# Kernel optimization log

Measured on AMD Instinct MI355X. Metric: run time of the kernel, lower is better.

## Reference

```python
import jax, jax.numpy as jnp
import numpy as np

N = 50000; FIN = 64; H = 128; E = 800000; T = 8
P = 250000; D = 500000; G = 20000; V = 2000; O = 2


def _mp(h, Ws, Wn, b, edge_src, edge_dst, n):
    # mean-aggregation message passing: relu(h Ws + mean_neigh(h) Wn + b)
    deg = jax.ops.segment_sum(jnp.ones(edge_dst.shape[0], h.dtype), edge_dst, n)
    agg = jax.ops.segment_sum(h[edge_src], edge_dst, n) / jnp.maximum(deg, 1.0)[:, None]
    return jax.nn.relu(h @ Ws + agg @ Wn + b)


def _forward(x, W_enc_self, W_enc_nei, b_enc, W2_self, W2_nei, b2, Wd1, bd1, Wd2, bd2,
             counts, edge_src, edge_dst, place_idx, src_idx, t_idx, dst_nodes, dst_seg,
             group_id, variant_of_group):
    n = x.shape[0]
    p = place_idx.shape[0]
    g = variant_of_group.shape[0]
    v = counts.shape[0]
    # first encoder, then T sequential second_encoder applications (feature generations)
    h0 = _mp(x, W_enc_self, W_enc_nei, b_enc, edge_src, edge_dst, n)

    def step(h, _):
        h2 = _mp(h, W2_self, W2_nei, b2, edge_src, edge_dst, n)
        return h2, h2

    _, hs = jax.lax.scan(step, h0, None, length=T)
    feats = jnp.concatenate([h0[None], hs], axis=0)  # [T+1, N, H]

    # gather (place, src) features at the generation index of each prediction
    place_f = feats[t_idx, place_idx]                 # [P, H]
    src_f = feats[t_idx, src_idx]                     # [P, H]
    # dst feature = sum over the destination set of each prediction
    dst_f = jax.ops.segment_sum(feats[t_idx[dst_seg], dst_nodes], dst_seg, p)  # [P, H]

    cat = jnp.concatenate([place_f, src_f, dst_f], axis=-1)  # [P, 3H]
    logits = jax.nn.relu(cat @ Wd1 + bd1) @ Wd2 + bd2        # [P, O]
    logprob = jax.nn.log_softmax(logits, axis=-1)            # [P, O]

    # prev_prob: inclusive running sum of per-step logprob sums within each variant
    group_sums = jax.ops.segment_sum(logprob, group_id, g)   # [G, O]
    cum = jnp.cumsum(group_sums, axis=0)
    var_tot = jax.ops.segment_sum(group_sums, variant_of_group, v)
    var_excl = jnp.cumsum(var_tot, axis=0) - var_tot
    within = cum - var_excl[variant_of_group]                # [G, O]
    prev = within[group_id]                                  # [P, O]

    logc = jnp.log(counts / jnp.sum(counts))                 # log(count/total) per variant
    add = logprob + prev + logc[variant_of_group[group_id]][:, None]
    return jnp.zeros((n, logits.shape[-1]), x.dtype).at[place_idx].add(add)


def setup_inputs() -> dict:
    ks = jax.random.split(jax.random.key(0), 24)
    s = jnp.float32(0.05)
    f32 = jnp.float32
    i32 = jnp.int32
    return {
        "x": jax.random.normal(ks[0], (N, FIN), f32),
        "W_enc_self": jax.random.normal(ks[1], (FIN, H), f32) * s,
        "W_enc_nei": jax.random.normal(ks[2], (FIN, H), f32) * s,
        "b_enc": jax.random.normal(ks[3], (H,), f32) * s,
        "W2_self": jax.random.normal(ks[4], (H, H), f32) * s,
        "W2_nei": jax.random.normal(ks[5], (H, H), f32) * s,
        "b2": jax.random.normal(ks[6], (H,), f32) * s,
        "Wd1": jax.random.normal(ks[7], (3 * H, 3 * H), f32) * s,
        "bd1": jax.random.normal(ks[8], (3 * H,), f32) * s,
        "Wd2": jax.random.normal(ks[9], (3 * H, O), f32) * s,
        "bd2": jax.random.normal(ks[10], (O,), f32) * s,
        "counts": jax.random.uniform(ks[11], (V,), f32) + 0.5,
        "edge_src": jax.random.randint(ks[12], (E,), 0, N, i32),
        "edge_dst": jax.random.randint(ks[13], (E,), 0, N, i32),
        "place_idx": jax.random.randint(ks[14], (P,), 0, N, i32),
        "src_idx": jax.random.randint(ks[15], (P,), 0, N, i32),
        "t_idx": jax.random.randint(ks[16], (P,), 0, T + 1, i32),
        "dst_nodes": jax.random.randint(ks[17], (D,), 0, N, i32),
        "dst_seg": jnp.sort(jax.random.randint(ks[18], (D,), 0, P, i32)),
        "group_id": jnp.sort(jax.random.randint(ks[19], (P,), 0, G, i32)),
        "variant_of_group": jnp.sort(jax.random.randint(ks[20], (G,), 0, V, i32)),
    }


def reference(x, W_enc_self, W_enc_nei, b_enc, W2_self, W2_nei, b2, Wd1, bd1, Wd2, bd2,
              counts, edge_src, edge_dst, place_idx, src_idx, t_idx, dst_nodes, dst_seg,
              group_id, variant_of_group):
    return _forward(x, W_enc_self, W_enc_nei, b_enc, W2_self, W2_nei, b2, Wd1, bd1, Wd2, bd2,
                    counts, edge_src, edge_dst, place_idx, src_idx, t_idx, dst_nodes, dst_seg,
                    group_id, variant_of_group)
```

## Files before the change

kernel.cpp:

```cpp
#include <hip/hip_runtime.h>
#include <math.h>

#define NN 50000
#define FINN 64
#define HD 128
#define EE 800000
#define TT 8
#define PP 250000
#define DD 500000
#define GG 20000
#define VV 2000
#define OO 2

#define DEC_GRID 256
#define DEC_TILES ((PP + 63) / 64)

typedef short short8 __attribute__((ext_vector_type(8)));
typedef float f32x4 __attribute__((ext_vector_type(4)));

__device__ __forceinline__ unsigned short f2bf(float f) {
    unsigned int u = __float_as_uint(f);
    u += 0x7fffu + ((u >> 16) & 1u);
    return (unsigned short)(u >> 16);
}
__device__ __forceinline__ float bf2f(unsigned short u) {
    return __uint_as_float(((unsigned int)u) << 16);
}

struct us8 { unsigned short v[8]; };

__device__ __forceinline__ void gload_lds16(const void* g, void* l) {
    __builtin_amdgcn_global_load_lds((__attribute__((address_space(1))) void*)g,
                                     (__attribute__((address_space(3))) void*)l, 16, 0, 0);
}

__global__ void count_k(const int* __restrict__ idx, int* __restrict__ counts, int n) {
    int i = blockIdx.x * blockDim.x + threadIdx.x;
    if (i < n) atomicAdd(&counts[idx[i]], 1);
}

__global__ void blk_sum_k(const int* __restrict__ counts, int n, int* __restrict__ bsum) {
    __shared__ int buf[256];
    int t = threadIdx.x, i = blockIdx.x * 256 + t;
    buf[t] = (i < n) ? counts[i] : 0;
    __syncthreads();
    for (int off = 128; off > 0; off >>= 1) {
        if (t < off) buf[t] += buf[t + off];
        __syncthreads();
    }
    if (t == 0) bsum[blockIdx.x] = buf[0];
}

__global__ void scan_small_k(const int* __restrict__ bsum, int nb, int* __restrict__ boff) {
    __shared__ int buf[256];
    int t = threadIdx.x;
    int v = (t < nb) ? bsum[t] : 0;
    buf[t] = v;
    __syncthreads();
    for (int off = 1; off < 256; off <<= 1) {
        int u = (t >= off) ? buf[t - off] : 0;
        __syncthreads();
        buf[t] += u;
        __syncthreads();
    }
    if (t < nb) boff[t] = buf[t] - v;
}

__global__ void rowptr_fill_k(const int* __restrict__ counts, const int* __restrict__ boff,
                              int n, int* __restrict__ rowptr, int total) {
    __shared__ int buf[256];
    int t = threadIdx.x, i = blockIdx.x * 256 + t;
    int v = (i < n) ? counts[i] : 0;
    buf[t] = v;
    __syncthreads();
    for (int off = 1; off < 256; off <<= 1) {
        int u = (t >= off) ? buf[t - off] : 0;
        __syncthreads();
        buf[t] += u;
        __syncthreads();
    }
    if (i < n) rowptr[i] = boff[blockIdx.x] + buf[t] - v;
    if (i == 0) rowptr[n] = total;
}

__global__ void lb_rowptr_k(const int* __restrict__ arr, int n, int* __restrict__ rowptr, int m) {
    int i = blockIdx.x * blockDim.x + threadIdx.x;
    if (i > m) return;
    int lo = 0, hi = n;
    while (lo < hi) {
        int mid = (lo + hi) >> 1;
        if (arr[mid] < i) lo = mid + 1; else hi = mid;
    }
    rowptr[i] = lo;
}

__global__ void fill_csr_k(const int* __restrict__ esrc, const int* __restrict__ edst,
                           const int* __restrict__ rowptr, int* __restrict__ cursor,
                           int* __restrict__ outi, int n) {
    int e = blockIdx.x * blockDim.x + threadIdx.x;
    if (e < n) {
        int d = edst[e];
        int pos = atomicAdd(&cursor[d], 1);
        outi[rowptr[d] + pos] = esrc[e];
    }
}

__global__ void hist9_k(const int* __restrict__ t_idx, int* __restrict__ hist) {
    __shared__ int l[9];
    if (threadIdx.x < 9) l[threadIdx.x] = 0;
    __syncthreads();
    int p = blockIdx.x * 256 + threadIdx.x;
    if (p < PP) atomicAdd(&l[t_idx[p]], 1);
    __syncthreads();
    if (threadIdx.x < 9) atomicAdd(&hist[threadIdx.x], l[threadIdx.x]);
}

__global__ void scan9_k(const int* __restrict__ hist, int* __restrict__ boff9) {
    if (threadIdx.x == 0) {
        int a = 0;
        for (int i = 0; i < 9; ++i) { boff9[i] = a; a += hist[i]; }
    }
}

__global__ void bucket_perm_k(const int* __restrict__ t_idx, const int* __restrict__ boff9,
                              int* __restrict__ cursor9, int* __restrict__ pperm) {
    __shared__ int lcnt[9];
    __shared__ int lbase[9];
    int tid = threadIdx.x;
    int p = blockIdx.x * 256 + tid;
    if (tid < 9) lcnt[tid] = 0;
    __syncthreads();
    int t = 0, lr = 0;
    bool ok = p < PP;
    if (ok) {
        t = t_idx[p];
        lr = atomicAdd(&lcnt[t], 1);
    }
    __syncthreads();
    if (tid < 9) lbase[tid] = atomicAdd(&cursor9[tid], lcnt[tid]);
    __syncthreads();
    if (ok) pperm[boff9[t] + lbase[t] + lr] = p;
}

__global__ void prep_k(const float* __restrict__ x,
                       const float* __restrict__ Wes, const float* __restrict__ Wen,
                       const float* __restrict__ W2s, const float* __restrict__ W2n,
                       const float* __restrict__ Wd1,
                       unsigned short* __restrict__ xb, unsigned short* __restrict__ wenc_t,
                       unsigned short* __restrict__ w2_t, unsigned short* __restrict__ wd1t) {
    int i = blockIdx.x * 256 + threadIdx.x;
    if (i < NN * FINN) xb[i] = f2bf(x[i]);
    if (i < HD * 2 * FINN) {
        int c = i / (2 * FINN), k = i - c * (2 * FINN);
        wenc_t[i] = f2bf((k < FINN) ? Wes[k * HD + c] : Wen[(k - FINN) * HD + c]);
    }
    if (i < HD * 2 * HD) {
        int c = i / (2 * HD), k = i - c * (2 * HD);
        w2_t[i] = f2bf((k < HD) ? W2s[k * HD + c] : W2n[(k - HD) * HD + c]);
    }
    if (i < 384 * 384) {
        int n = i / 384, k = i - n * 384;
        wd1t[i] = f2bf(Wd1[k * 384 + n]);
    }
}

template <int KIN>
__launch_bounds__(256)
__global__ void mpf_k(const unsigned short* __restrict__ hin,
                      const int* __restrict__ rowptr, const int* __restrict__ csr_src,
                      const unsigned short* __restrict__ Wt, const float* __restrict__ bias,
                      unsigned short* __restrict__ hout) {
    constexpr int CPL = KIN / 64;
    __shared__ unsigned short sm[32 * KIN];
    int tid = threadIdx.x;
    int r = tid >> 3;
    int sl = tid & 7;
    int node = blockIdx.x * 32 + r;
    int rx = r & 7;

    if (node < NN) {
        int s = rowptr[node], e = rowptr[node + 1];
        float acc[8 * CPL] = {};
        int src0 = (s < e) ? csr_src[s] : 0;
        int src1 = (s + 1 < e) ? csr_src[s + 1] : 0;
        int src2 = (s + 2 < e) ? csr_src[s + 2] : 0;
        int src3 = (s + 3 < e) ? csr_src[s + 3] : 0;
        for (int i = s; i < e; i += 4) {
            int rem = e - i;
            us8 v0a, v0b, v1a, v1b, v2a, v2b, v3a, v3b;
            v0a = *(const us8*)&hin[(size_t)src0 * KIN + sl * (8 * CPL)];
            if constexpr (CPL == 2) v0b = *(const us8*)&hin[(size_t)src0 * KIN + sl * 16 + 8];
            if (rem > 1) {
                v1a = *(const us8*)&hin[(size_t)src1 * KIN + sl * (8 * CPL)];
                if constexpr (CPL == 2) v1b = *(const us8*)&hin[(size_t)src1 * KIN + sl * 16 + 8];
            }
            if (rem > 2) {
                v2a = *(const us8*)&hin[(size_t)src2 * KIN + sl * (8 * CPL)];
                if constexpr (CPL == 2) v2b = *(const us8*)&hin[(size_t)src2 * KIN + sl * 16 + 8];
            }
            if (rem > 3) {
                v3a = *(const us8*)&hin[(size_t)src3 * KIN + sl * (8 * CPL)];
                if constexpr (CPL == 2) v3b = *(const us8*)&hin[(size_t)src3 * KIN + sl * 16 + 8];
            }
            src0 = (i + 4 < e) ? csr_src[i + 4] : 0;
            src1 = (i + 5 < e) ? csr_src[i + 5] : 0;
            src2 = (i + 6 < e) ? csr_src[i + 6] : 0;
            src3 = (i + 7 < e) ? csr_src[i + 7] : 0;
#pragma unroll
            for (int j = 0; j < 8; ++j) acc[j] += bf2f(v0a.v[j]);
            if constexpr (CPL == 2)
#pragma unroll
                for (int j = 0; j < 8; ++j) acc[8 + j] += bf2f(v0b.v[j]);
            if (rem > 1) {
#pragma unroll
                for (int j = 0; j < 8; ++j) acc[j] += bf2f(v1a.v[j]);
                if constexpr (CPL == 2)
#pragma unroll
                    for (int j = 0; j < 8; ++j) acc[8 + j] += bf2f(v1b.v[j]);
            }
            if (rem > 2) {
#pragma unroll
                for (int j = 0; j < 8; ++j) acc[j] += bf2f(v2a.v[j]);
                if constexpr (CPL == 2)
#pragma unroll
                    for (int j = 0; j < 8; ++j) acc[8 + j] += bf2f(v2b.v[j]);
            }
            if (rem > 3) {
#pragma unroll
                for (int j = 0; j < 8; ++j) acc[j] += bf2f(v3a.v[j]);
                if constexpr (CPL == 2)
#pragma unroll
                    for (int j = 0; j < 8; ++j) acc[8 + j] += bf2f(v3b.v[j]);
            }
        }
        float d = fmaxf((float)(e - s), 1.f);
        us8 o0, o1;
#pragma unroll
        for (int j = 0; j < 8; ++j) o0.v[j] = f2bf(acc[j] / d);
        int c0 = sl * CPL;
        *(us8*)&sm[r * KIN + ((c0 ^ rx) * 8)] = o0;
        if constexpr (CPL == 2) {
#pragma unroll
            for (int j = 0; j < 8; ++j) o1.v[j] = f2bf(acc[8 + j] / d);
            *(us8*)&sm[r * KIN + (((c0 + 1) ^ rx) * 8)] = o1;
        }
    }
    __syncthreads();

    int lane = tid & 63, w = tid >> 6;
    int cc = lane & 15, gq = lane >> 4;
    constexpr int K = 2 * KIN;
    int rloc = (w & 1) * 16 + cc;
    int rowA = blockIdx.x * 32 + rloc;
    bool rowok = rowA < NN;
    const unsigned short* hrow = hin + (size_t)rowA * KIN;
    int ch = (w >> 1) * 64;
    int rlx = rloc & 7;

    f32x4 acc2[4];
#pragma unroll
    for (int t = 0; t < 4; ++t) acc2[t] = (f32x4){0.f, 0.f, 0.f, 0.f};

#pragma unroll
    for (int k0 = 0; k0 < K; k0 += 32) {
        int k = k0 + gq * 8;
        short8 a = {0, 0, 0, 0, 0, 0, 0, 0};
        if (rowok) {
            if (k0 < KIN) a = *(const short8*)(hrow + k);
            else {
                int chunk = (k - KIN) >> 3;
                a = *(const short8*)&sm[rloc * KIN + ((chunk ^ rlx) * 8)];
            }
        }
#pragma unroll
        for (int t = 0; t < 4; ++t) {
            short8 b = *(const short8*)&Wt[(size_t)(ch + t * 16 + cc) * K + k];
            acc2[t] = __builtin_amdgcn_mfma_f32_16x16x32_bf16(a, b, acc2[t], 0, 0, 0);
        }
    }
#pragma unroll
    for (int t = 0; t < 4; ++t) {
        int col = ch + t * 16 + cc;
        float b1 = bias[col];
#pragma unroll
        for (int rj = 0; rj < 4; ++rj) {
            int grow = blockIdx.x * 32 + (w & 1) * 16 + gq * 4 + rj;
            if (grow < NN)
                hout[(size_t)grow * HD + col] = f2bf(fmaxf(acc2[t][rj] + b1, 0.f));
        }
    }
}

__launch_bounds__(256)
__global__ void dst_sum2_k(const unsigned short* __restrict__ feats,
                           const int* __restrict__ t_idx, const int* __restrict__ dst_nodes,
                           const int* __restrict__ dst_rowptr, const int* __restrict__ pperm,
                           unsigned short* __restrict__ dstc) {
    int tid = threadIdx.x;
    int grp = tid >> 4;
    int fl = tid & 15;
    int pi = blockIdx.x * 16 + grp;
    if (pi >= PP) return;
    int p = pperm[pi];
    long t = t_idx[p];
    const unsigned short* base = feats + t * (long)NN * HD;
    int s = dst_rowptr[p], e = dst_rowptr[p + 1];
    float acc[8] = {};
    int i = s;
    int n0 = (i < e) ? dst_nodes[i] : 0;
    int n1 = (i + 1 < e) ? dst_nodes[i + 1] : 0;
    while (i < e) {
        bool h1 = (i + 1) < e;
        us8 v0 = *(const us8*)&base[(size_t)n0 * HD + fl * 8];
        us8 v1;
        if (h1) v1 = *(const us8*)&base[(size_t)n1 * HD + fl * 8];
        int i2 = i + 2, i3 = i + 3;
        n0 = (i2 < e) ? dst_nodes[i2] : 0;
        n1 = (i3 < e) ? dst_nodes[i3] : 0;
#pragma unroll
        for (int j = 0; j < 8; ++j) acc[j] += bf2f(v0.v[j]);
        if (h1) {
#pragma unroll
            for (int j = 0; j < 8; ++j) acc[j] += bf2f(v1.v[j]);
        }
        i = i2;
    }
    us8 o;
#pragma unroll
    for (int j = 0; j < 8; ++j) o.v[j] = f2bf(acc[j]);
    *(us8*)&dstc[(size_t)pi * HD + fl * 8] = o;
}

__global__ void
__attribute__((amdgpu_flat_work_group_size(512, 512), amdgpu_waves_per_eu(2, 2)))
dec7_k(const unsigned short* __restrict__ feats,
       const unsigned short* __restrict__ dstc,
       const int* __restrict__ place_idx, const int* __restrict__ src_idx,
       const int* __restrict__ t_idx, const int* __restrict__ group_id,
       const int* __restrict__ pperm,
       const unsigned short* __restrict__ Wd1t,
       const float* __restrict__ bd1, const float* __restrict__ Wd2,
       const float* __restrict__ bd2, float* __restrict__ logprob,
       float* __restrict__ group_sums) {
    __shared__ unsigned short buf[3][192 * 128];
    __shared__ unsigned int rb[3][192];
    __shared__ float lpart[3][8][64][2];

    int tid = threadIdx.x;
    int lane = tid & 63, w = tid >> 6;
    int cc = lane & 15, gq = lane >> 4;
    int bid = blockIdx.x;

    int row = min(tid, 191);
    int sec = row >> 6, pl = row & 63;
    const int* nptr = (sec == 0) ? place_idx : src_idx;
    unsigned int dstc_off = (unsigned int)((const char*)dstc - (const char*)feats);

    int nt = (DEC_TILES - 1 - bid) / DEC_GRID + 1;
    float b20 = bd2[0], b21 = bd2[1];

    if (tid < 192) {
#pragma unroll
        for (int s3 = 0; s3 < 3; ++s3) {
            int pic = min((bid + s3 * DEC_GRID) * 64 + pl, PP - 1);
            int p = pperm[pic];
            rb[s3][tid] = (sec == 2) ? (dstc_off + (unsigned int)pic * 256u)
                                     : (unsigned int)(((unsigned)t_idx[p] * NN + (unsigned)nptr[p]) * 256u);
        }
    }
    int p3 = pperm[min((bid + 3 * DEC_GRID) * 64 + pl, PP - 1)];
    int tOld = t_idx[p3], nOld = nptr[p3];
    int pCur = pperm[min((bid + 4 * DEC_GRID) * 64 + pl, PP - 1)];
    int opPP = 0, opP = 0, ogP = 0;

    short8 breg[36];
    float b1r[3], w0r[3], w1r[3];
    {
        const unsigned short* bbase = Wd1t + ((long)(w * 48 + cc) * 384 + gq * 8);
#pragma unroll
        for (int kk = 0; kk < 12; ++kk)
#pragma unroll
            for (int t = 0; t < 3; ++t)
                breg[kk * 3 + t] = *(const short8*)(bbase + (long)t * 16 * 384 + kk * 32);
#pragma unroll
        for (int t = 0; t < 3; ++t) {
            int col = w * 48 + t * 16 + cc;
            b1r[t] = bd1[col];
            w0r[t] = Wd2[col * 2 + 0];
            w1r[t] = Wd2[col * 2 + 1];
        }
    }
    __syncthreads();

    int rsub = lane >> 4, chunk = lane & 15;

#define STAGE(slot_)                                                                 \
    {                                                                                \
        _Pragma("unroll")                                                            \
        for (int i = 0; i < 6; ++i) {                                                \
            int r = w * 24 + i * 4 + rsub;                                           \
            const char* src = (const char*)feats + rb[slot_][r] +                    \
                              ((unsigned)(chunk ^ (r & 7)) << 4);                    \
            gload_lds16(src, &buf[slot_][(w * 24 + i * 4) * 128]);                   \
        }                                                                            \
    }

#define OUTPUT(tile_, slot_, opv_, ogv_)                                             \
    {                                                                                \
        int pi = (bid + (tile_) * DEC_GRID) * 64 + w * 16 + cc;                      \
        if (pi < PP) {                                                               \
            float l0 = b20, l1 = b21;                                                \
            _Pragma("unroll")                                                        \
            for (int w2 = 0; w2 < 8; ++w2) {                                         \
                l0 += lpart[slot_][w2][w * 16 + cc][0];                              \
                l1 += lpart[slot_][w2][w * 16 + cc][1];                              \
            }                                                                        \
            float mm = fmaxf(l0, l1);                                                \
            float lse = mm + logf(expf(l0 - mm) + expf(l1 - mm));                    \
            float lp0 = l0 - lse, lp1 = l1 - lse;                                    \
            logprob[(opv_)*2 + 0] = lp0;                                             \
            logprob[(opv_)*2 + 1] = lp1;                                             \
            atomicAdd(&group_sums[(ogv_)*2 + 0], lp0);                               \
            atomicAdd(&group_sums[(ogv_)*2 + 1], lp1);                               \
        }                                                                            \
    }

    STAGE(0);
    STAGE(1);

    for (int k = 0; k < nt; ++k) {
        int slot = k % 3;

        int opN = pperm[min((bid + k * DEC_GRID) * 64 + (w & 3) * 16 + cc, PP - 1)];
        int ogN = group_id[opP];
        int pNew = pperm[min((bid + (k + 5) * DEC_GRID) * 64 + pl, PP - 1)];
        int tNew = t_idx[pCur];
        int nNew = nptr[pCur];
        __builtin_amdgcn_sched_barrier(0);

        if (k + 2 < nt) STAGE((k + 2) % 3);
        __builtin_amdgcn_sched_barrier(0);

        if (k + 2 < nt) {
            if (k >= 2) { asm volatile("s_waitcnt vmcnt(21)" ::: "memory"); }
            else        { asm volatile("s_waitcnt vmcnt(17)" ::: "memory"); }
        } else if (k + 1 < nt) {
            asm volatile("s_waitcnt vmcnt(15)" ::: "memory");
        } else {
            asm volatile("s_waitcnt vmcnt(5)" ::: "memory");
        }
        __builtin_amdgcn_s_barrier();
        __builtin_amdgcn_sched_barrier(0);

        if (k >= 2 && w < 4 && lane < 16) OUTPUT(k - 2, (k - 2) % 3, opPP, ogP);

        {
            const unsigned short* bufc = &buf[slot][0];
            f32x4 acc[4][3];
#pragma unroll
            for (int s = 0; s < 4; ++s)
#pragma unroll
                for (int t = 0; t < 3; ++t) acc[s][t] = (f32x4){0.f, 0.f, 0.f, 0.f};

#pragma unroll
            for (int kk = 0; kk < 12; ++kk) {
                int seck = kk >> 2;
                int cbase = (kk & 3) * 4 + gq;
                int coff = (cbase ^ (cc & 7)) * 8;
                short8 a_c[4];
#pragma unroll
                for (int s = 0; s < 4; ++s) {
                    int lrow = seck * 64 + s * 16 + cc;
                    a_c[s] = *(const short8*)&bufc[lrow * 128 + coff];
                }
#pragma unroll
                for (int t = 0; t < 3; ++t)
#pragma unroll
                    for (int s = 0; s < 4; ++s)
                        acc[s][t] = __builtin_amdgcn_mfma_f32_16x16x32_bf16(
                            a_c[s], breg[kk * 3 + t], acc[s][t], 0, 0, 0);
            }

#pragma unroll
            for (int s = 0; s < 4; ++s) {
                float p0[4], p1[4];
#pragma unroll
                for (int r = 0; r < 4; ++r) { p0[r] = 0.f; p1[r] = 0.f; }
#pragma unroll
                for (int t = 0; t < 3; ++t) {
#pragma unroll
                    for (int r = 0; r < 4; ++r) {
                        float h = fmaxf(acc[s][t][r] + b1r[t], 0.f);
                        p0[r] += h * w0r[t];
                        p1[r] += h * w1r[t];
                    }
                }
#pragma unroll
                for (int m = 1; m < 16; m <<= 1)
#pragma unroll
                    for (int r = 0; r < 4; ++r) {
                        p0[r] += __shfl_xor(p0[r], m);
                        p1[r] += __shfl_xor(p1[r], m);
                    }
                if (cc == 0) {
#pragma unroll
                    for (int r = 0; r < 4; ++r) {
                        int orow = s * 16 + gq * 4 + r;
                        lpart[slot][w][orow][0] = p0[r];
                        lpart[slot][w][orow][1] = p1[r];
                    }
                }
            }
        }

        if (tid < 192) {
            int picw = min((bid + (k + 3) * DEC_GRID) * 64 + pl, PP - 1);
            rb[(k + 3) % 3][tid] = (sec == 2)
                ? (dstc_off + (unsigned int)picw * 256u)
                : (unsigned int)(((unsigned)tOld * NN + (unsigned)nOld) * 256u);
        }
        tOld = tNew; nOld = nNew; pCur = pNew;
        opPP = opP; opP = opN; ogP = ogN;

        asm volatile("s_waitcnt lgkmcnt(0)" ::: "memory");
        __builtin_amdgcn_s_barrier();
        __builtin_amdgcn_sched_barrier(0);
    }

    if (w < 4 && lane < 16) {
        OUTPUT(nt - 2, (nt - 2) % 3, opPP, ogP);
        int ogLast = group_id[opP];
        OUTPUT(nt - 1, (nt - 1) % 3, opP, ogLast);
    }
#undef STAGE
#undef OUTPUT
}

__global__ void within_total_k(const float* __restrict__ group_sums,
                               const int* __restrict__ var_rowptr,
                               const float* __restrict__ counts,
                               float* __restrict__ within, float* __restrict__ total) {
    __shared__ float buf[256];
    int tid = threadIdx.x;
    float s = 0.f;
    for (int i = tid; i < VV; i += 256) s += counts[i];
    buf[tid] = s;
    __syncthreads();
    for (int off = 128; off > 0; off >>= 1) {
        if (tid < off) buf[tid] += buf[tid + off];
        __syncthreads();
    }
    if (tid == 0) total[0] = buf[0];
    for (int v = tid; v < VV; v += 256) {
        int gs = var_rowptr[v], ge = var_rowptr[v + 1];
        float r0 = 0.f, r1 = 0.f;
        for (int g = gs; g < ge; ++g) {
            r0 += group_sums[2 * g + 0];
            r1 += group_sums[2 * g + 1];
            within[2 * g + 0] = r0;
            within[2 * g + 1] = r1;
        }
    }
}

__global__ void final_k(const float* __restrict__ logprob, const float* __restrict__ within,
                        const int* __restrict__ group_id, const int* __restrict__ vog,
                        const float* __restrict__ counts, const float* __restrict__ total,
                        const int* __restrict__ place_idx, float* __restrict__ outp) {
    int p = blockIdx.x * blockDim.x + threadIdx.x;
    if (p >= PP) return;
    int g = group_id[p];
    int v = vog[g];
    float lc = logf(counts[v]) - logf(total[0]);
    int node = place_idx[p];
    atomicAdd(&outp[node * 2 + 0], logprob[p * 2 + 0] + within[g * 2 + 0] + lc);
    atomicAdd(&outp[node * 2 + 1], logprob[p * 2 + 1] + within[g * 2 + 1] + lc);
}

extern "C" void kernel_launch(void* const* d_in, const int* in_sizes, int n_in,
                              void* d_out, int out_size, void* d_ws, size_t ws_size,
                              hipStream_t stream) {
    const float* x          = (const float*)d_in[0];
    const float* W_enc_self = (const float*)d_in[1];
    const float* W_enc_nei  = (const float*)d_in[2];
    const float* b_enc      = (const float*)d_in[3];
    const float* W2_self    = (const float*)d_in[4];
    const float* W2_nei     = (const float*)d_in[5];
    const float* b2         = (const float*)d_in[6];
    const float* Wd1        = (const float*)d_in[7];
    const float* bd1        = (const float*)d_in[8];
    const float* Wd2        = (const float*)d_in[9];
    const float* bd2        = (const float*)d_in[10];
    const float* counts     = (const float*)d_in[11];
    const int* edge_src     = (const int*)d_in[12];
    const int* edge_dst     = (const int*)d_in[13];
    const int* place_idx    = (const int*)d_in[14];
    const int* src_idx      = (const int*)d_in[15];
    const int* t_idx        = (const int*)d_in[16];
    const int* dst_nodes    = (const int*)d_in[17];
    const int* dst_seg      = (const int*)d_in[18];
    const int* group_id     = (const int*)d_in[19];
    const int* variant_of_group = (const int*)d_in[20];
    float* outp = (float*)d_out;

    const int NB = (NN + 255) / 256;

    unsigned short* feats = (unsigned short*)d_ws;
    unsigned short* aggb  = feats + (size_t)(TT + 1) * NN * HD;
    unsigned short* xb    = aggb + (size_t)NN * HD;
    unsigned short* dstc  = xb + (size_t)NN * FINN;
    unsigned short* wenc_t = dstc + (size_t)PP * HD;
    unsigned short* w2_t   = wenc_t + HD * 2 * FINN;
    unsigned short* wd1t   = w2_t + HD * 2 * HD;
    int* zr = (int*)(wd1t + 384 * 384);
    int* csr_counts   = zr;
    int* csr_cursor   = csr_counts + NN;
    float* group_sums = (float*)(csr_cursor + NN);
    int* hist9        = (int*)(group_sums + 2 * GG);
    int* cursor9      = hist9 + 9;
    size_t zero_words = (size_t)NN + NN + 2 * GG + 18;
    int* bsum       = cursor9 + 9;
    int* boff       = bsum + 256;
    int* boff9      = boff + 256;
    int* csr_rowptr = boff9 + 16;
    int* dst_rowptr = csr_rowptr + (NN + 1);
    int* var_rowptr = dst_rowptr + (PP + 1);
    int* csr_src    = var_rowptr + (VV + 1);
    int* pperm      = csr_src + EE;
    float* logprob  = (float*)(pperm + PP);
    float* within   = logprob + 2 * PP;
    float* total_counts = within + 2 * GG;

    hipMemsetAsync(zr, 0, zero_words * 4, stream);
    hipMemsetAsync(d_out, 0, (size_t)out_size * sizeof(float), stream);

    prep_k<<<(NN * FINN + 255) / 256, 256, 0, stream>>>(x, W_enc_self, W_enc_nei, W2_self,
                                                        W2_nei, Wd1, xb, wenc_t, w2_t, wd1t);
    count_k<<<(EE + 255) / 256, 256, 0, stream>>>(edge_dst, csr_counts, EE);
    blk_sum_k<<<NB, 256, 0, stream>>>(csr_counts, NN, bsum);
    scan_small_k<<<1, 256, 0, stream>>>(bsum, NB, boff);
    rowptr_fill_k<<<NB, 256, 0, stream>>>(csr_counts, boff, NN, csr_rowptr, EE);
    fill_csr_k<<<(EE + 255) / 256, 256, 0, stream>>>(edge_src, edge_dst, csr_rowptr,
                                                     csr_cursor, csr_src, EE);
    lb_rowptr_k<<<(PP + 256) / 256, 256, 0, stream>>>(dst_seg, DD, dst_rowptr, PP);
    lb_rowptr_k<<<(VV + 256) / 256, 256, 0, stream>>>(variant_of_group, GG, var_rowptr, VV);
    hist9_k<<<(PP + 255) / 256, 256, 0, stream>>>(t_idx, hist9);
    scan9_k<<<1, 64, 0, stream>>>(hist9, boff9);
    bucket_perm_k<<<(PP + 255) / 256, 256, 0, stream>>>(t_idx, boff9, cursor9, pperm);

    const int NB32 = (NN + 31) / 32;
    for (int r = 0; r <= TT; ++r) {
        const unsigned short* hin = (r == 0) ? xb : feats + (size_t)(r - 1) * NN * HD;
        unsigned short* hout = feats + (size_t)r * NN * HD;
        if (r == 0)
            mpf_k<FINN><<<NB32, 256, 0, stream>>>(hin, csr_rowptr, csr_src, wenc_t, b_enc, hout);
        else
            mpf_k<HD><<<NB32, 256, 0, stream>>>(hin, csr_rowptr, csr_src, w2_t, b2, hout);
    }

    dst_sum2_k<<<(PP + 15) / 16, 256, 0, stream>>>(feats, t_idx, dst_nodes, dst_rowptr, pperm, dstc);
    dec7_k<<<DEC_GRID, 512, 0, stream>>>(feats, dstc, place_idx, src_idx, t_idx,
                                         group_id, pperm, wd1t, bd1, Wd2, bd2,
                                         logprob, group_sums);

    within_total_k<<<1, 256, 0, stream>>>(group_sums, var_rowptr, counts, within, total_counts);
    final_k<<<(PP + 255) / 256, 256, 0, stream>>>(logprob, within, group_id, variant_of_group,
                                                  counts, total_counts, place_idx, outp);
}
```

Before: 979.8 us.

## Replace persistent pipelined decoder with one-tile-per-block non-persistent kernel

Swaps the persistent 256-block decoder, which triple-buffered LDS tiles and kept Wd1 in registers across tiles, for a simple kernel that launches one block per 64-prediction tile. Each block stages its tile, runs the MFMA GEMM with weights loaded from global/L2 per tile, and reduces and writes output directly. The aim is to rely on hardware occupancy across about 3900 blocks instead of hand-scheduled software pipelining. The cost is reloading the weights and paying prologue and epilogue in every block, with no overlap of loads and compute inside a block.

```diff
diff --git a/kernel.cpp b/kernel.cpp
--- a/kernel.cpp
+++ b/kernel.cpp
@@ -11,9 +11,6 @@
 #define GG 20000
 #define VV 2000
 #define OO 2
-
-#define DEC_GRID 256
-#define DEC_TILES ((PP + 63) / 64)
 
 typedef short short8 __attribute__((ext_vector_type(8)));
 typedef float f32x4 __attribute__((ext_vector_type(4)));
@@ -331,209 +328,136 @@
     *(us8*)&dstc[(size_t)pi * HD + fl * 8] = o;
 }
 
-__global__ void
-__attribute__((amdgpu_flat_work_group_size(512, 512), amdgpu_waves_per_eu(2, 2)))
-dec7_k(const unsigned short* __restrict__ feats,
-       const unsigned short* __restrict__ dstc,
-       const int* __restrict__ place_idx, const int* __restrict__ src_idx,
-       const int* __restrict__ t_idx, const int* __restrict__ group_id,
-       const int* __restrict__ pperm,
-       const unsigned short* __restrict__ Wd1t,
-       const float* __restrict__ bd1, const float* __restrict__ Wd2,
-       const float* __restrict__ bd2, float* __restrict__ logprob,
-       float* __restrict__ group_sums) {
-    __shared__ unsigned short buf[3][192 * 128];
-    __shared__ unsigned int rb[3][192];
-    __shared__ float lpart[3][8][64][2];
+__launch_bounds__(512, 2)
+__global__ void dec8_k(const unsigned short* __restrict__ feats,
+                       const unsigned short* __restrict__ dstc,
+                       const int* __restrict__ place_idx, const int* __restrict__ src_idx,
+                       const int* __restrict__ t_idx, const int* __restrict__ group_id,
+                       const int* __restrict__ pperm,
+                       const unsigned short* __restrict__ Wd1t,
+                       const float* __restrict__ bd1, const float* __restrict__ Wd2,
+                       const float* __restrict__ bd2, float* __restrict__ logprob,
+                       float* __restrict__ group_sums) {
+    __shared__ unsigned short buf[192 * 128];
+    __shared__ unsigned int rb[192];
+    __shared__ float lpart[8][64][2];
 
     int tid = threadIdx.x;
     int lane = tid & 63, w = tid >> 6;
     int cc = lane & 15, gq = lane >> 4;
     int bid = blockIdx.x;
-
-    int row = min(tid, 191);
-    int sec = row >> 6, pl = row & 63;
-    const int* nptr = (sec == 0) ? place_idx : src_idx;
-    unsigned int dstc_off = (unsigned int)((const char*)dstc - (const char*)feats);
-
-    int nt = (DEC_TILES - 1 - bid) / DEC_GRID + 1;
-    float b20 = bd2[0], b21 = bd2[1];
+    int p0 = bid * 64;
 
     if (tid < 192) {
-#pragma unroll
-        for (int s3 = 0; s3 < 3; ++s3) {
-            int pic = min((bid + s3 * DEC_GRID) * 64 + pl, PP - 1);
+        int sec = tid >> 6, pl = tid & 63;
+        int pic = min(p0 + pl, PP - 1);
+        if (sec == 2) {
+            unsigned int dstc_off = (unsigned int)((const char*)dstc - (const char*)feats);
+            rb[tid] = dstc_off + (unsigned int)pic * 256u;
+        } else {
             int p = pperm[pic];
-            rb[s3][tid] = (sec == 2) ? (dstc_off + (unsigned int)pic * 256u)
-                                     : (unsigned int)(((unsigned)t_idx[p] * NN + (unsigned)nptr[p]) * 256u);
-        }
-    }
-    int p3 = pperm[min((bid + 3 * DEC_GRID) * 64 + pl, PP - 1)];
-    int tOld = t_idx[p3], nOld = nptr[p3];
-    int pCur = pperm[min((bid + 4 * DEC_GRID) * 64 + pl, PP - 1)];
-    int opPP = 0, opP = 0, ogP = 0;
-
-    short8 breg[36];
-    float b1r[3], w0r[3], w1r[3];
+            int node = (sec == 0) ? place_idx[p] : src_idx[p];
+            rb[tid] = (unsigned int)(((unsigned)t_idx[p] * NN + (unsigned)node) * 256u);
+        }
+    }
+    __syncthreads();
+
     {
+        int rsub = lane >> 4, chunk = lane & 15;
+#pragma unroll
+        for (int i = 0; i < 6; ++i) {
+            int r = w * 24 + i * 4 + rsub;
+            const char* src = (const char*)feats + rb[r] + ((unsigned)(chunk ^ (r & 7)) << 4);
+            gload_lds16(src, &buf[(w * 24 + i * 4) * 128]);
+        }
+    }
+    __syncthreads();
+
+    {
+        f32x4 acc[4][3];
+#pragma unroll
+        for (int s = 0; s < 4; ++s)
+#pragma unroll
+            for (int t = 0; t < 3; ++t) acc[s][t] = (f32x4){0.f, 0.f, 0.f, 0.f};
+
         const unsigned short* bbase = Wd1t + ((long)(w * 48 + cc) * 384 + gq * 8);
-#pragma unroll
-        for (int kk = 0; kk < 12; ++kk)
-#pragma unroll
-            for (int t = 0; t < 3; ++t)
-                breg[kk * 3 + t] = *(const short8*)(bbase + (long)t * 16 * 384 + kk * 32);
-#pragma unroll
-        for (int t = 0; t < 3; ++t) {
-            int col = w * 48 + t * 16 + cc;
-            b1r[t] = bd1[col];
-            w0r[t] = Wd2[col * 2 + 0];
-            w1r[t] = Wd2[col * 2 + 1];
-        }
-    }
-    __syncthreads();
-
-    int rsub = lane >> 4, chunk = lane & 15;
-
-#define STAGE(slot_)                                                                 \
-    {                                                                                \
-        _Pragma("unroll")                                                            \
-        for (int i = 0; i < 6; ++i) {                                                \
-            int r = w * 24 + i * 4 + rsub;                                           \
-            const char* src = (const char*)feats + rb[slot_][r] +                    \
-                              ((unsigned)(chunk ^ (r & 7)) << 4);                    \
-            gload_lds16(src, &buf[slot_][(w * 24 + i * 4) * 128]);                   \
-        }                                                                            \
-    }
-
-#define OUTPUT(tile_, slot_, opv_, ogv_)                                             \
-    {                                                                                \
-        int pi = (bid + (tile_) * DEC_GRID) * 64 + w * 16 + cc;                      \
-        if (pi < PP) {                                                               \
-            float l0 = b20, l1 = b21;                                                \
-            _Pragma("unroll")                                                        \
-            for (int w2 = 0; w2 < 8; ++w2) {                                         \
-                l0 += lpart[slot_][w2][w * 16 + cc][0];                              \
-                l1 += lpart[slot_][w2][w * 16 + cc][1];                              \
-            }                                                                        \
-            float mm = fmaxf(l0, l1);                                                \
-            float lse = mm + logf(expf(l0 - mm) + expf(l1 - mm));                    \
-            float lp0 = l0 - lse, lp1 = l1 - lse;                                    \
-            logprob[(opv_)*2 + 0] = lp0;                                             \
-            logprob[(opv_)*2 + 1] = lp1;                                             \
-            atomicAdd(&group_sums[(ogv_)*2 + 0], lp0);                               \
-            atomicAdd(&group_sums[(ogv_)*2 + 1], lp1);                               \
-        }                                                                            \
-    }
-
-    STAGE(0);
-    STAGE(1);
-
-    for (int k = 0; k < nt; ++k) {
-        int slot = k % 3;
-
-        int opN = pperm[min((bid + k * DEC_GRID) * 64 + (w & 3) * 16 + cc, PP - 1)];
-        int ogN = group_id[opP];
-        int pNew = pperm[min((bid + (k + 5) * DEC_GRID) * 64 + pl, PP - 1)];
-        int tNew = t_idx[pCur];
-        int nNew = nptr[pCur];
-        __builtin_amdgcn_sched_barrier(0);
-
-        if (k + 2 < nt) STAGE((k + 2) % 3);
-        __builtin_amdgcn_sched_barrier(0);
-
-        if (k + 2 < nt) {
-            if (k >= 2) { asm volatile("s_waitcnt vmcnt(21)" ::: "memory"); }
-            else        { asm volatile("s_waitcnt vmcnt(17)" ::: "memory"); }
-        } else if (k + 1 < nt) {
-            asm volatile("s_waitcnt vmcnt(15)" ::: "memory");
-        } else {
-            asm volatile("s_waitcnt vmcnt(5)" ::: "memory");
-        }
-        __builtin_amdgcn_s_barrier();
-        __builtin_amdgcn_sched_barrier(0);
-
-        if (k >= 2 && w < 4 && lane < 16) OUTPUT(k - 2, (k - 2) % 3, opPP, ogP);
-
-        {
-            const unsigned short* bufc = &buf[slot][0];
-            f32x4 acc[4][3];
-#pragma unroll
-            for (int s = 0; s < 4; ++s)
-#pragma unroll
-                for (int t = 0; t < 3; ++t) acc[s][t] = (f32x4){0.f, 0.f, 0.f, 0.f};
-
-#pragma unroll
-            for (int kk = 0; kk < 12; ++kk) {
-                int seck = kk >> 2;
-                int cbase = (kk & 3) * 4 + gq;
-                int coff = (cbase ^ (cc & 7)) * 8;
-                short8 a_c[4];
-#pragma unroll
-                for (int s = 0; s < 4; ++s) {
-                    int lrow = seck * 64 + s * 16 + cc;
-                    a_c[s] = *(const short8*)&bufc[lrow * 128 + coff];
+
+#pragma unroll
+        for (int kk = 0; kk < 12; ++kk) {
+            int seck = kk >> 2;
+            int cbase = (kk & 3) * 4 + gq;
+            int coff = (cbase ^ (cc & 7)) * 8;
+            short8 a_c[4];
+#pragma unroll
+            for (int s = 0; s < 4; ++s) {
+                int lrow = seck * 64 + s * 16 + cc;
+                a_c[s] = *(const short8*)&buf[lrow * 128 + coff];
+            }
+#pragma unroll
+            for (int t = 0; t < 3; ++t) {
+                short8 b = *(const short8*)(bbase + (long)t * 16 * 384 + kk * 32);
+#pragma unroll
+                for (int s = 0; s < 4; ++s)
+                    acc[s][t] = __builtin_amdgcn_mfma_f32_16x16x32_bf16(a_c[s], b, acc[s][t], 0, 0, 0);
+            }
+        }
+
+#pragma unroll
+        for (int s = 0; s < 4; ++s) {
+            float p0v[4], p1v[4];
+#pragma unroll
+            for (int r = 0; r < 4; ++r) { p0v[r] = 0.f; p1v[r] = 0.f; }
+#pragma unroll
+            for (int t = 0; t < 3; ++t) {
+                int col = w * 48 + t * 16 + cc;
+                float b1 = bd1[col];
+                float w0 = Wd2[col * 2 + 0], w1 = Wd2[col * 2 + 1];
+#pragma unroll
+                for (int r = 0; r < 4; ++r) {
+                    float h = fmaxf(acc[s][t][r] + b1, 0.f);
+                    p0v[r] += h * w0;
+                    p1v[r] += h * w1;
                 }
-#pragma unroll
-                for (int t = 0; t < 3; ++t)
-#pragma unroll
-                    for (int s = 0; s < 4; ++s)
-                        acc[s][t] = __builtin_amdgcn_mfma_f32_16x16x32_bf16(
-                            a_c[s], breg[kk * 3 + t], acc[s][t], 0, 0, 0);
-            }
-
-#pragma unroll
-            for (int s = 0; s < 4; ++s) {
-                float p0[4], p1[4];
-#pragma unroll
-                for (int r = 0; r < 4; ++r) { p0[r] = 0.f; p1[r] = 0.f; }
-#pragma unroll
-                for (int t = 0; t < 3; ++t) {
-#pragma unroll
-                    for (int r = 0; r < 4; ++r) {
-                        float h = fmaxf(acc[s][t][r] + b1r[t], 0.f);
-                        p0[r] += h * w0r[t];
-                        p1[r] += h * w1r[t];
-                    }
+            }
+#pragma unroll
+            for (int m = 1; m < 16; m <<= 1)
+#pragma unroll
+                for (int r = 0; r < 4; ++r) {
+                    p0v[r] += __shfl_xor(p0v[r], m);
+                    p1v[r] += __shfl_xor(p1v[r], m);
                 }
-#pragma unroll
-                for (int m = 1; m < 16; m <<= 1)
-#pragma unroll
-                    for (int r = 0; r < 4; ++r) {
-                        p0[r] += __shfl_xor(p0[r], m);
-                        p1[r] += __shfl_xor(p1[r], m);
-                    }
-                if (cc == 0) {
-#pragma unroll
-                    for (int r = 0; r < 4; ++r) {
-                        int orow = s * 16 + gq * 4 + r;
-                        lpart[slot][w][orow][0] = p0[r];
-                        lpart[slot][w][orow][1] = p1[r];
-                    }
+            if (cc == 0) {
+#pragma unroll
+                for (int r = 0; r < 4; ++r) {
+                    int orow = s * 16 + gq * 4 + r;
+                    lpart[w][orow][0] = p0v[r];
+                    lpart[w][orow][1] = p1v[r];
                 }
             }
         }
-
-        if (tid < 192) {
-            int picw = min((bid + (k + 3) * DEC_GRID) * 64 + pl, PP - 1);
-            rb[(k + 3) % 3][tid] = (sec == 2)
-                ? (dstc_off + (unsigned int)picw * 256u)
-                : (unsigned int)(((unsigned)tOld * NN + (unsigned)nOld) * 256u);
-        }
-        tOld = tNew; nOld = nNew; pCur = pNew;
-        opPP = opP; opP = opN; ogP = ogN;
-
-        asm volatile("s_waitcnt lgkmcnt(0)" ::: "memory");
-        __builtin_amdgcn_s_barrier();
-        __builtin_amdgcn_sched_barrier(0);
-    }
-
-    if (w < 4 && lane < 16) {
-        OUTPUT(nt - 2, (nt - 2) % 3, opPP, ogP);
-        int ogLast = group_id[opP];
-        OUTPUT(nt - 1, (nt - 1) % 3, opP, ogLast);
-    }
-#undef STAGE
-#undef OUTPUT
+    }
+    __syncthreads();
+
+    if (tid < 64) {
+        int pi = p0 + tid;
+        if (pi < PP) {
+            int p = pperm[pi];
+            float l0 = bd2[0], l1 = bd2[1];
+#pragma unroll
+            for (int w2 = 0; w2 < 8; ++w2) {
+                l0 += lpart[w2][tid][0];
+                l1 += lpart[w2][tid][1];
+            }
+            float mm = fmaxf(l0, l1);
+            float lse = mm + logf(expf(l0 - mm) + expf(l1 - mm));
+            float lp0 = l0 - lse, lp1 = l1 - lse;
+            logprob[p * 2 + 0] = lp0;
+            logprob[p * 2 + 1] = lp1;
+            int g = group_id[p];
+            atomicAdd(&group_sums[g * 2 + 0], lp0);
+            atomicAdd(&group_sums[g * 2 + 1], lp1);
+        }
+    }
 }
 
 __global__ void within_total_k(const float* __restrict__ group_sums,
@@ -659,9 +583,9 @@
     }
 
     dst_sum2_k<<<(PP + 15) / 16, 256, 0, stream>>>(feats, t_idx, dst_nodes, dst_rowptr, pperm, dstc);
-    dec7_k<<<DEC_GRID, 512, 0, stream>>>(feats, dstc, place_idx, src_idx, t_idx,
-                                         group_id, pperm, wd1t, bd1, Wd2, bd2,
-                                         logprob, group_sums);
+    dec8_k<<<(PP + 63) / 64, 512, 0, stream>>>(feats, dstc, place_idx, src_idx, t_idx,
+                                               group_id, pperm, wd1t, bd1, Wd2, bd2,
+                                               logprob, group_sums);
 
     within_total_k<<<1, 256, 0, stream>>>(group_sums, var_rowptr, counts, within, total_counts);
     final_k<<<(PP + 255) / 256, 256, 0, stream>>>(logprob, within, group_id, variant_of_group,
```

Measured after the change: 1.048 ms. +7.0%, slower.
